# Performance work log

Hardware: AMD Instinct MI355X
Metric: run time of the kernel (lower is better)

## Reference

```python
import jax, jax.numpy as jnp
import numpy as np

IMG, PATCH, DIM, DEPTH, HEADS = 224, 16, 768, 12, 12
GRID = IMG // PATCH            # 14 patches per side
NPATCH = GRID * GRID           # 196
N = NPATCH + 1                 # 197 tokens incl. cls
HD = DIM // HEADS              # 64
NRD = (2 * GRID - 1) ** 2 + 3  # 732 relative-distance entries (incl. 3 cls slots)
FF = 4 * DIM                   # 3072
BATCH = 32


def _rel_pos_index():
    # Faithful port of the torch buffer construction (with_cls_token=True).
    coords = np.stack(np.meshgrid(np.arange(GRID), np.arange(GRID), indexing='ij'))
    cf = coords.reshape(2, -1)                                   # [2, 196]
    rel = (cf[:, :, None] - cf[:, None, :]).transpose(1, 2, 0)   # [196,196,2]
    rel = rel.astype(np.int64)
    rel[:, :, 0] += GRID - 1
    rel[:, :, 1] += GRID - 1
    rel[:, :, 0] *= 2 * GRID - 1
    rpi = np.zeros((N, N), dtype=np.int32)
    rpi[1:, 1:] = rel.sum(-1)
    rpi[0, :] = NRD - 3
    rpi[:, 0] = NRD - 2
    rpi[0, 0] = NRD - 1
    return jnp.asarray(rpi)

RPI = _rel_pos_index()  # [197,197] int32, constant


def layernorm(x, w, b, eps=1e-5):
    mu = x.mean(-1, keepdims=True)
    var = x.var(-1, keepdims=True)  # biased, like torch LayerNorm
    return (x - mu) * jax.lax.rsqrt(var + eps) * w + b


def setup_inputs() -> dict:
    key = jax.random.key(0)
    ks = jax.random.split(key, 12)
    s = 0.02
    f32 = jnp.float32
    return {
        'x': jax.random.normal(ks[0], (BATCH, 3, IMG, IMG), f32),
        # PatchEmbed conv (stride == kernel) expressed as a matmul weight.
        'patch_w': jax.random.normal(ks[1], (DIM, 3 * PATCH * PATCH), f32) * s,
        'patch_b': jnp.zeros((DIM,), f32),
        'cls_token': jax.random.normal(ks[2], (1, 1, DIM), f32) * s,
        # Per-block params, stacked along depth for lax.scan.
        'norm1_w': jnp.ones((DEPTH, DIM), f32),
        'norm1_b': jnp.zeros((DEPTH, DIM), f32),
        'qkv_w': jax.random.normal(ks[3], (DEPTH, 3 * DIM, DIM), f32) * s,
        'q_bias': jax.random.normal(ks[4], (DEPTH, DIM), f32) * s,
        'v_bias': jax.random.normal(ks[5], (DEPTH, DIM), f32) * s,
        'rpb_table': jax.random.normal(ks[6], (DEPTH, NRD, HEADS), f32) * s,
        'proj_w': jax.random.normal(ks[7], (DEPTH, DIM, DIM), f32) * s,
        'proj_b': jnp.zeros((DEPTH, DIM), f32),
        'norm2_w': jnp.ones((DEPTH, DIM), f32),
        'norm2_b': jnp.zeros((DEPTH, DIM), f32),
        'fc1_w': jax.random.normal(ks[8], (DEPTH, FF, DIM), f32) * s,
        'fc1_b': jnp.zeros((DEPTH, FF), f32),
        'fc2_w': jax.random.normal(ks[9], (DEPTH, DIM, FF), f32) * s,
        'fc2_b': jnp.zeros((DEPTH, DIM), f32),
        'normf_w': jnp.ones((DIM,), f32),
        'normf_b': jnp.zeros((DIM,), f32),
    }


def reference(x, patch_w, patch_b, cls_token, norm1_w, norm1_b, qkv_w, q_bias, v_bias,
              rpb_table, proj_w, proj_b, norm2_w, norm2_b, fc1_w, fc1_b, fc2_w, fc2_b,
              normf_w, normf_b):
    B = x.shape[0]
    # Patch embed: stride==kernel conv == patchify + matmul.
    p = x.reshape(B, 3, GRID, PATCH, GRID, PATCH).transpose(0, 2, 4, 1, 3, 5)
    p = p.reshape(B, NPATCH, 3 * PATCH * PATCH)
    tokens = p @ patch_w.T + patch_b                              # [B,196,768]
    tokens = jnp.concatenate([jnp.broadcast_to(cls_token, (B, 1, DIM)), tokens], axis=1)
    scale = HD ** -0.5

    def block(h, params):
        (n1w, n1b, qw, qb, vb, rpt, pw, pb, n2w, n2b, f1w, f1b, f2w, f2b) = params
        y = layernorm(h, n1w, n1b)
        bias = jnp.concatenate([qb, jnp.zeros_like(vb), vb])      # k bias is zero
        qkv = (y @ qw.T + bias).reshape(B, N, 3, HEADS, HD).transpose(2, 0, 3, 1, 4)
        q, k, v = qkv[0] * scale, qkv[1], qkv[2]                  # [B,H,N,HD]
        attn = jnp.einsum('bhnd,bhmd->bhnm', q, k)                # [B,H,N,N]
        rpb = rpt[RPI]                                            # [N,N,H] gather
        attn = attn + rpb.transpose(2, 0, 1)[None]
        attn = jax.nn.softmax(attn, axis=-1)
        o = jnp.einsum('bhnm,bhmd->bnhd', attn, v).reshape(B, N, DIM)
        h = h + o @ pw.T + pb
        y = layernorm(h, n2w, n2b)
        y = jax.nn.gelu(y @ f1w.T + f1b, approximate=False)       # torch nn.GELU (erf)
        h = h + y @ f2w.T + f2b
        return h, None

    params = (norm1_w, norm1_b, qkv_w, q_bias, v_bias, rpb_table, proj_w, proj_b,
              norm2_w, norm2_b, fc1_w, fc1_b, fc2_w, fc2_b)
    tokens, _ = jax.lax.scan(block, tokens, params)
    return layernorm(tokens, normf_w, normf_b)                    # [B,197,768]
```

## Files before the change

kernel.cpp:

```cpp
#include <hip/hip_runtime.h>
#include <hip/hip_bf16.h>


#define B_     32
#define DIM_   768
#define N_     197
#define M_     (B_*N_)
#define NP_    196
#define MP_    (B_*NP_)
#define HEADS_ 12
#define HD_    64
#define FF_    3072
#define NRD_   732
#define QKV_   2304
#define DEPTH_ 12

typedef unsigned short u16;
typedef unsigned int   u32;
typedef __attribute__((ext_vector_type(4))) float    f32x4;
typedef __attribute__((ext_vector_type(8))) u16      ushort8;
typedef __attribute__((ext_vector_type(8))) __bf16   bf16x8;

__device__ __forceinline__ float b2f(u16 u) {
    return __builtin_bit_cast(float, ((u32)u) << 16);
}
__device__ __forceinline__ u16 f2b(float f) {
    u32 u = __builtin_bit_cast(u32, f);
    u32 r = u + 0x7fffu + ((u >> 16) & 1u);
    return (u16)(r >> 16);
}
__device__ __forceinline__ float lo16(u32 v) { return __builtin_bit_cast(float, v << 16); }
__device__ __forceinline__ float hi16(u32 v) { return __builtin_bit_cast(float, v & 0xffff0000u); }

__device__ __forceinline__ f32x4 mfma16(ushort8 a, ushort8 b, f32x4 c) {
    return __builtin_amdgcn_mfma_f32_16x16x32_bf16(
        __builtin_bit_cast(bf16x8, a), __builtin_bit_cast(bf16x8, b), c, 0, 0, 0);
}

__device__ __forceinline__ void gload16(const u16* g, u16* lds) {
    __builtin_amdgcn_global_load_lds(
        (const __attribute__((address_space(1))) void*)g,
        (__attribute__((address_space(3))) void*)lds, 16, 0, 0);
}

__global__ void cvt_k(const float* __restrict__ src, u16* __restrict__ dst, int n8) {
    int g = blockIdx.x * 256 + threadIdx.x;
    if (g >= n8) return;
    size_t o = (size_t)g * 8;
    float4 f0 = *(const float4*)(src + o);
    float4 f1 = *(const float4*)(src + o + 4);
    ushort8 r;
    r[0]=f2b(f0.x); r[1]=f2b(f0.y); r[2]=f2b(f0.z); r[3]=f2b(f0.w);
    r[4]=f2b(f1.x); r[5]=f2b(f1.y); r[6]=f2b(f1.z); r[7]=f2b(f1.w);
    *(ushort8*)(dst + o) = r;
}

#define SEG0 1769472
#define SEG1 589824
#define SEG2 2359296
#define SEG3 2359296
__global__ void cvt4_k(const float* __restrict__ s0, const float* __restrict__ s1,
                       const float* __restrict__ s2, const float* __restrict__ s3,
                       u16* __restrict__ dst) {
    int g = blockIdx.x * 256 + threadIdx.x;
    if (g >= (SEG0+SEG1+SEG2+SEG3)/8) return;
    size_t o = (size_t)g * 8;
    const float* src; size_t lo_;
    if (o < SEG0)             { src = s0; lo_ = o; }
    else if (o < SEG0+SEG1)   { src = s1; lo_ = o - SEG0; }
    else if (o < (size_t)SEG0+SEG1+SEG2) { src = s2; lo_ = o - SEG0 - SEG1; }
    else                      { src = s3; lo_ = o - SEG0 - SEG1 - SEG2; }
    float4 f0 = *(const float4*)(src + lo_);
    float4 f1 = *(const float4*)(src + lo_ + 4);
    ushort8 r;
    r[0]=f2b(f0.x); r[1]=f2b(f0.y); r[2]=f2b(f0.z); r[3]=f2b(f0.w);
    r[4]=f2b(f1.x); r[5]=f2b(f1.y); r[6]=f2b(f1.z); r[7]=f2b(f1.w);
    *(ushort8*)(dst + o) = r;
}

__global__ void patchify_k(const float* __restrict__ X, u16* __restrict__ P) {
    int idx = blockIdx.x * 256 + threadIdx.x;
    if (idx >= MP_ * DIM_) return;
    int row = idx / DIM_, k = idx - row * DIM_;
    int b = row / NP_, p = row - b * NP_;
    int gy = p / 14, gx = p - gy * 14;
    int c = k >> 8, r = k & 255;
    int py = r >> 4, px = r & 15;
    P[idx] = f2b(X[((b * 3 + c) * 224 + gy * 16 + py) * 224 + gx * 16 + px]);
}

__global__ void build_tokens_k(const float* __restrict__ P, const float* __restrict__ cls,
                               float* __restrict__ T) {
    int idx = blockIdx.x * 256 + threadIdx.x;
    if (idx >= M_ * DIM_) return;
    int row = idx / DIM_, c = idx - row * DIM_;
    int b = row / N_, t = row - b * N_;
    T[idx] = (t == 0) ? cls[c] : P[(size_t)(b * NP_ + t - 1) * DIM_ + c];
}

__global__ void qkvbias_all_k(const float* __restrict__ qb, const float* __restrict__ vb,
                              float* __restrict__ out) {
    int g = blockIdx.x * 256 + threadIdx.x;
    if (g >= DEPTH_ * QKV_) return;
    int l = g / QKV_, n = g - l * QKV_;
    out[g] = (n < DIM_) ? qb[l * DIM_ + n]
                        : (n < 2 * DIM_ ? 0.f : vb[l * DIM_ + n - 2 * DIM_]);
}

template <int OUTBF>
__global__ void layernorm_k(const float* __restrict__ X, const float* __restrict__ w,
                            const float* __restrict__ bta, void* __restrict__ Yv) {
    int row = blockIdx.x;
    const float* x = X + (size_t)row * DIM_;
    int t = threadIdx.x;
    float v[3]; float s = 0.f, q = 0.f;
#pragma unroll
    for (int i = 0; i < 3; i++) { float u = x[t + i * 256]; v[i] = u; s += u; q += u * u; }
#pragma unroll
    for (int off = 32; off > 0; off >>= 1) {
        s += __shfl_down(s, off, 64);
        q += __shfl_down(q, off, 64);
    }
    __shared__ float ss[4], qq[4];
    int wid = t >> 6, lane = t & 63;
    if (!lane) { ss[wid] = s; qq[wid] = q; }
    __syncthreads();
    s = ss[0] + ss[1] + ss[2] + ss[3];
    q = qq[0] + qq[1] + qq[2] + qq[3];
    float mu = s * (1.f / 768.f);
    float var = q * (1.f / 768.f) - mu * mu;
    float rs = rsqrtf(var + 1e-5f);
#pragma unroll
    for (int i = 0; i < 3; i++) {
        int c = t + i * 256;
        float o = (v[i] - mu) * rs * w[c] + bta[c];
        if (OUTBF) ((u16*)Yv)[(size_t)row * DIM_ + c] = f2b(o);
        else       ((float*)Yv)[(size_t)row * DIM_ + c] = o;
    }
}

template <int ACT, int OUTBF>
__launch_bounds__(512)
__global__ void gemm_bt(const u16* __restrict__ A, const u16* __restrict__ W,
                        const float* __restrict__ bias, const float* res,
                        void* Cv, int M, int Nc, int K) {
    __shared__ u16 As[2][128 * 32];
    __shared__ u16 Ws[2][128 * 32];
    const int tid = threadIdx.x;
    const int lane = tid & 63, w = tid >> 6;
    const int llo = lane & 15, lhi = lane >> 4;
    const int wm = w & 3, wn = w >> 2;

    const int nwg = gridDim.x * gridDim.y;
    int bid = blockIdx.y * gridDim.x + blockIdx.x;
    {
        int q = nwg >> 3, r = nwg & 7;
        int xcd = bid & 7, idx = bid >> 3;
        bid = (xcd < r ? xcd * (q + 1) : r * (q + 1) + (xcd - r) * q) + idx;
    }
    const int m0 = (bid / gridDim.x) * 128, n0 = (bid % gridDim.x) * 128;

    f32x4 acc[2][4] = {};

    const int srow = tid >> 2, scol = (tid & 3) * 8;
    int ar = m0 + srow; if (ar >= M) ar = M - 1;
    const u16* ga = A + (size_t)ar * K + scol;
    const u16* gw = W + (size_t)(n0 + srow) * K + scol;
    const int ldso = (w * 16) * 32;

    gload16(ga, As[0] + ldso);
    gload16(gw, Ws[0] + ldso);
    __syncthreads();

    int cur = 0;
    for (int k0 = 32; k0 < K; k0 += 32) {
        const int nxt = cur ^ 1;
        gload16(ga + k0, As[nxt] + ldso);
        gload16(gw + k0, Ws[nxt] + ldso);
        ushort8 af[2], bfr[4];
#pragma unroll
        for (int mi = 0; mi < 2; mi++)
            af[mi] = *(const ushort8*)(As[cur] + (wm * 32 + mi * 16 + llo) * 32 + lhi * 8);
#pragma unroll
        for (int ni = 0; ni < 4; ni++)
            bfr[ni] = *(const ushort8*)(Ws[cur] + (wn * 64 + ni * 16 + llo) * 32 + lhi * 8);
#pragma unroll
        for (int mi = 0; mi < 2; mi++)
#pragma unroll
            for (int ni = 0; ni < 4; ni++)
                acc[mi][ni] = mfma16(af[mi], bfr[ni], acc[mi][ni]);
        __syncthreads();
        cur = nxt;
    }
    {
        ushort8 af[2], bfr[4];
#pragma unroll
        for (int mi = 0; mi < 2; mi++)
            af[mi] = *(const ushort8*)(As[cur] + (wm * 32 + mi * 16 + llo) * 32 + lhi * 8);
#pragma unroll
        for (int ni = 0; ni < 4; ni++)
            bfr[ni] = *(const ushort8*)(Ws[cur] + (wn * 64 + ni * 16 + llo) * 32 + lhi * 8);
#pragma unroll
        for (int mi = 0; mi < 2; mi++)
#pragma unroll
            for (int ni = 0; ni < 4; ni++)
                acc[mi][ni] = mfma16(af[mi], bfr[ni], acc[mi][ni]);
    }
    const int cb = n0 + wn * 64 + llo;
    const int rb = m0 + wm * 32 + lhi * 4;
#pragma unroll
    for (int ni = 0; ni < 4; ni++) {
        int col = cb + ni * 16;
        float bv = bias ? bias[col] : 0.f;
#pragma unroll
        for (int mi = 0; mi < 2; mi++) {
#pragma unroll
            for (int rg = 0; rg < 4; rg++) {
                int row = rb + mi * 16 + rg;
                if (row >= M) continue;
                float t = acc[mi][ni][rg] + bv;
                if (ACT) t = 0.5f * t * (1.f + erff(t * 0.70710678118654752f));
                if (res) t += res[(size_t)row * Nc + col];
                if (OUTBF) ((u16*)Cv)[(size_t)row * Nc + col] = f2b(t);
                else       ((float*)Cv)[(size_t)row * Nc + col] = t;
            }
        }
    }
}

__device__ __forceinline__ int vswz(int d) {
    return ((d & 7) ^ ((d >> 3) & 7)) << 3;
}

__launch_bounds__(256)
__global__ void attn3_k(const u16* __restrict__ qkv, const float* __restrict__ rpt,
                        u16* __restrict__ O) {
    __shared__ u16 smem[16128 + 16384];
    u16* Ks = smem;
    u16* Vt = smem + 16128;
    u16* Ps = smem;
    const int b = blockIdx.x / HEADS_, hh = blockIdx.x % HEADS_;
    const int i0 = blockIdx.y * 64;
    const int t = threadIdx.x;
    const int w = t >> 6, lane = t & 63;
    const int lhi = lane >> 4, llo = lane & 15;
    const size_t base = (size_t)b * N_ * QKV_ + (size_t)hh * HD_;
    const int iw = i0 + w * 16;

    int qrow = iw + llo; if (qrow > 196) qrow = 196;
    const ushort8 af0 = *(const ushort8*)(qkv + base + (size_t)qrow * QKV_ + lhi * 8);
    const ushort8 af1 = *(const ushort8*)(qkv + base + (size_t)qrow * QKV_ + 32 + lhi * 8);

    for (int g = t; g < 1576; g += 256) {
        int j = g >> 3, d0 = (g & 7) * 8;
        ushort8 kv = *(const ushort8*)(qkv + base + (size_t)j * QKV_ + 768 + d0);
        *(ushort8*)(Ks + j * 72 + d0) = kv;
        ushort8 vv = *(const ushort8*)(qkv + base + (size_t)j * QKV_ + 1536 + d0);
#pragma unroll
        for (int e = 0; e < 8; e++) {
            int d = d0 + e;
            Vt[d * 256 + (j ^ vswz(d))] = ((const u16*)&vv)[e];
        }
    }
    if (t < 216) {
        int j = 197 + (t >> 3), d0 = (t & 7) * 8;
        *(uint4*)(Ks + j * 72 + d0) = make_uint4(0u, 0u, 0u, 0u);
    }
    for (int g = t; g < 1728; g += 256) {
        int d = g / 27, c = 197 + (g - d * 27);
        Vt[d * 256 + (c ^ vswz(d))] = 0;
    }
    __syncthreads();

    const bool wvalid = (iw <= 196);
    f32x4 acc[14] = {};
    float mx[4], sum[4];

    if (wvalid) {
#pragma unroll
        for (int jt = 0; jt < 14; jt++) {
            const u16* kp = Ks + (jt * 16 + llo) * 72 + lhi * 8;
            ushort8 b0 = *(const ushort8*)(kp);
            ushort8 b1 = *(const ushort8*)(kp + 32);
            acc[jt] = mfma16(af0, b0, acc[jt]);
            acc[jt] = mfma16(af1, b1, acc[jt]);
        }
        int iy4[4], ix4[4]; bool icls[4];
#pragma unroll
        for (int rg = 0; rg < 4; rg++) {
            int i = iw + lhi * 4 + rg; if (i > 196) i = 196;
            icls[rg] = (i == 0);
            int pi = i - 1;
            iy4[rg] = pi / 14; ix4[rg] = pi - iy4[rg] * 14;
            mx[rg] = -INFINITY;
        }
#pragma unroll
        for (int jt = 0; jt < 14; jt++) {
            int j = jt * 16 + llo;
            if (j <= 196) {
                bool jcls = (j == 0);
                int pj = j - 1;
                int jy = pj / 14, jx = pj - jy * 14;
#pragma unroll
                for (int rg = 0; rg < 4; rg++) {
                    int idx;
                    if (icls[rg])  idx = jcls ? (NRD_ - 1) : (NRD_ - 3);
                    else if (jcls) idx = NRD_ - 2;
                    else           idx = (iy4[rg] - jy + 13) * 27 + (ix4[rg] - jx + 13);
                    float sv = acc[jt][rg] * 0.125f + rpt[idx * HEADS_ + hh];
                    acc[jt][rg] = sv;
                    mx[rg] = fmaxf(mx[rg], sv);
                }
            } else {
#pragma unroll
                for (int rg = 0; rg < 4; rg++) acc[jt][rg] = -INFINITY;
            }
        }
#pragma unroll
        for (int rg = 0; rg < 4; rg++) {
#pragma unroll
            for (int off = 1; off < 16; off <<= 1)
                mx[rg] = fmaxf(mx[rg], __shfl_xor(mx[rg], off, 64));
            sum[rg] = 0.f;
        }
#pragma unroll
        for (int jt = 0; jt < 14; jt++)
#pragma unroll
            for (int rg = 0; rg < 4; rg++) {
                float ev = __expf(acc[jt][rg] - mx[rg]);
                acc[jt][rg] = ev;
                sum[rg] += ev;
            }
#pragma unroll
        for (int rg = 0; rg < 4; rg++) {
#pragma unroll
            for (int off = 1; off < 16; off <<= 1)
                sum[rg] += __shfl_xor(sum[rg], off, 64);
            sum[rg] = 1.f / sum[rg];
        }
#pragma unroll
        for (int jt = 0; jt < 14; jt++)
#pragma unroll
            for (int rg = 0; rg < 4; rg++) acc[jt][rg] *= sum[rg];
    }
    __syncthreads();

    if (wvalid) {
#pragma unroll
        for (int jt = 0; jt < 14; jt++)
#pragma unroll
            for (int rg = 0; rg < 4; rg++)
                Ps[(w * 16 + lhi * 4 + rg) * 232 + jt * 16 + llo] = f2b(acc[jt][rg]);
        f32x4 o[4] = {};
#pragma unroll
        for (int jk = 0; jk < 7; jk++) {
            ushort8 pa = *(const ushort8*)(Ps + (w * 16 + llo) * 232 + jk * 32 + lhi * 8);
#pragma unroll
            for (int dt = 0; dt < 4; dt++) {
                int d = dt * 16 + llo;
                ushort8 vf = *(const ushort8*)(Vt + d * 256 + ((jk * 32 + lhi * 8) ^ vswz(d)));
                o[dt] = mfma16(pa, vf, o[dt]);
            }
        }
#pragma unroll
        for (int dt = 0; dt < 4; dt++)
#pragma unroll
            for (int rg = 0; rg < 4; rg++) {
                int i = iw + lhi * 4 + rg;
                if (i <= 196)
                    O[(size_t)(b * N_ + i) * DIM_ + hh * HD_ + dt * 16 + llo] = f2b(o[dt][rg]);
            }
    }
}

extern "C" void kernel_launch(void* const* d_in, const int* in_sizes, int n_in,
                              void* d_out, int out_size, void* d_ws, size_t ws_size,
                              hipStream_t stream) {
    (void)in_sizes; (void)n_in; (void)out_size; (void)ws_size;
    const float* x    = (const float*)d_in[0];
    const float* pew  = (const float*)d_in[1];
    const float* peb  = (const float*)d_in[2];
    const float* cls  = (const float*)d_in[3];
    const float* n1w  = (const float*)d_in[4];
    const float* n1b  = (const float*)d_in[5];
    const float* qkvw = (const float*)d_in[6];
    const float* qb   = (const float*)d_in[7];
    const float* vb   = (const float*)d_in[8];
    const float* rpt  = (const float*)d_in[9];
    const float* pw   = (const float*)d_in[10];
    const float* pb   = (const float*)d_in[11];
    const float* n2w  = (const float*)d_in[12];
    const float* n2b  = (const float*)d_in[13];
    const float* f1w  = (const float*)d_in[14];
    const float* f1b  = (const float*)d_in[15];
    const float* f2w  = (const float*)d_in[16];
    const float* f2b_ = (const float*)d_in[17];
    const float* nfw  = (const float*)d_in[18];
    const float* nfb  = (const float*)d_in[19];

    float* ws = (float*)d_ws;
    float* h     = ws;
    u16*   y     = (u16*)(ws + 4841472);
    float* un    = ws + 4841472 + 2420736;
    u16*   wbuf  = (u16*)(un + 9682944);
    float* qbias = (float*)(wbuf + 7077888);
    u16*   qkvb   = (u16*)un;
    u16*   hidden = (u16*)un;
    u16*   pmat   = (u16*)un;
    float* pout   = un + 4816896;

    const int MT = (M_ + 127) / 128;

    cvt_k<<<288, 256, 0, stream>>>(pew, wbuf, SEG1 / 8);
    patchify_k<<<(MP_ * DIM_ + 255) / 256, 256, 0, stream>>>(x, pmat);
    qkvbias_all_k<<<(DEPTH_ * QKV_ + 255) / 256, 256, 0, stream>>>(qb, vb, qbias);
    gemm_bt<0, 0><<<dim3(6, 49), 512, 0, stream>>>(pmat, wbuf, peb, nullptr, pout,
                                                   MP_, DIM_, DIM_);
    build_tokens_k<<<(M_ * DIM_ + 255) / 256, 256, 0, stream>>>(pout, cls, h);

    for (int l = 0; l < 12; l++) {
        layernorm_k<1><<<M_, 256, 0, stream>>>(h, n1w + l * DIM_, n1b + l * DIM_, y);
        cvt4_k<<<3456, 256, 0, stream>>>(qkvw + (size_t)l * SEG0, pw + (size_t)l * SEG1,
                                         f1w + (size_t)l * SEG2, f2w + (size_t)l * SEG3, wbuf);
        gemm_bt<0, 1><<<dim3(18, MT), 512, 0, stream>>>(y, wbuf, qbias + l * QKV_, nullptr,
                                                        qkvb, M_, QKV_, DIM_);
        attn3_k<<<dim3(384, 4), 256, 0, stream>>>(qkvb, rpt + (size_t)l * NRD_ * HEADS_, y);
        gemm_bt<0, 0><<<dim3(6, MT), 512, 0, stream>>>(y, wbuf + SEG0, pb + l * DIM_, h, h,
                                                       M_, DIM_, DIM_);
        layernorm_k<1><<<M_, 256, 0, stream>>>(h, n2w + l * DIM_, n2b + l * DIM_, y);
        gemm_bt<1, 1><<<dim3(24, MT), 512, 0, stream>>>(y, wbuf + SEG0 + SEG1, f1b + l * FF_,
                                                        nullptr, hidden, M_, FF_, DIM_);
        gemm_bt<0, 0><<<dim3(6, MT), 512, 0, stream>>>(hidden, wbuf + SEG0 + SEG1 + SEG2,
                                                       f2b_ + l * DIM_, h, h, M_, DIM_, FF_);
    }
    layernorm_k<0><<<M_, 256, 0, stream>>>(h, nfw, nfb, d_out);
}
```

Measured before the change: 3.573 ms.

## Deepen GEMM LDS pipeline to four stages and swizzle LDS layout

```diff
diff --git a/kernel.cpp b/kernel.cpp
--- a/kernel.cpp
+++ b/kernel.cpp
@@ -144,8 +144,8 @@
 __global__ void gemm_bt(const u16* __restrict__ A, const u16* __restrict__ W,
                         const float* __restrict__ bias, const float* res,
                         void* Cv, int M, int Nc, int K) {
-    __shared__ u16 As[2][128 * 32];
-    __shared__ u16 Ws[2][128 * 32];
+    __shared__ u16 As[4][128 * 32];
+    __shared__ u16 Ws[4][128 * 32];
     const int tid = threadIdx.x;
     const int lane = tid & 63, w = tid >> 6;
     const int llo = lane & 15, lhi = lane >> 4;
@@ -162,50 +162,50 @@
 
     f32x4 acc[2][4] = {};
 
-    const int srow = tid >> 2, scol = (tid & 3) * 8;
+    const int srow = tid >> 2;
+    const int scol = ((tid & 3) ^ ((srow >> 1) & 3)) * 8;
     int ar = m0 + srow; if (ar >= M) ar = M - 1;
     const u16* ga = A + (size_t)ar * K + scol;
     const u16* gw = W + (size_t)(n0 + srow) * K + scol;
     const int ldso = (w * 16) * 32;
 
-    gload16(ga, As[0] + ldso);
-    gload16(gw, Ws[0] + ldso);
-    __syncthreads();
-
-    int cur = 0;
-    for (int k0 = 32; k0 < K; k0 += 32) {
-        const int nxt = cur ^ 1;
-        gload16(ga + k0, As[nxt] + ldso);
-        gload16(gw + k0, Ws[nxt] + ldso);
+    const int rslot = (lhi ^ ((llo >> 1) & 3)) * 8;
+
+    const int nt = K >> 5;
+
+#pragma unroll
+    for (int p = 0; p < 3; ++p) {
+        gload16(ga + p * 32, As[p] + ldso);
+        gload16(gw + p * 32, Ws[p] + ldso);
+    }
+
+    for (int t = 0; t < nt; ++t) {
+        if (t < nt - 2)      asm volatile("s_waitcnt vmcnt(4)" ::: "memory");
+        else if (t < nt - 1) asm volatile("s_waitcnt vmcnt(2)" ::: "memory");
+        else                 asm volatile("s_waitcnt vmcnt(0)" ::: "memory");
+        __builtin_amdgcn_s_barrier();
+
+        const u16* ab = As[t & 3];
+        const u16* wb = Ws[t & 3];
         ushort8 af[2], bfr[4];
 #pragma unroll
         for (int mi = 0; mi < 2; mi++)
-            af[mi] = *(const ushort8*)(As[cur] + (wm * 32 + mi * 16 + llo) * 32 + lhi * 8);
+            af[mi] = *(const ushort8*)(ab + (wm * 32 + mi * 16 + llo) * 32 + rslot);
 #pragma unroll
         for (int ni = 0; ni < 4; ni++)
-            bfr[ni] = *(const ushort8*)(Ws[cur] + (wn * 64 + ni * 16 + llo) * 32 + lhi * 8);
+            bfr[ni] = *(const ushort8*)(wb + (wn * 64 + ni * 16 + llo) * 32 + rslot);
 #pragma unroll
         for (int mi = 0; mi < 2; mi++)
 #pragma unroll
             for (int ni = 0; ni < 4; ni++)
                 acc[mi][ni] = mfma16(af[mi], bfr[ni], acc[mi][ni]);
-        __syncthreads();
-        cur = nxt;
-    }
-    {
-        ushort8 af[2], bfr[4];
-#pragma unroll
-        for (int mi = 0; mi < 2; mi++)
-            af[mi] = *(const ushort8*)(As[cur] + (wm * 32 + mi * 16 + llo) * 32 + lhi * 8);
-#pragma unroll
-        for (int ni = 0; ni < 4; ni++)
-            bfr[ni] = *(const ushort8*)(Ws[cur] + (wn * 64 + ni * 16 + llo) * 32 + lhi * 8);
-#pragma unroll
-        for (int mi = 0; mi < 2; mi++)
-#pragma unroll
-            for (int ni = 0; ni < 4; ni++)
-                acc[mi][ni] = mfma16(af[mi], bfr[ni], acc[mi][ni]);
-    }
+
+        if (t + 3 < nt) {
+            gload16(ga + (size_t)(t + 3) * 32, As[(t + 3) & 3] + ldso);
+            gload16(gw + (size_t)(t + 3) * 32, Ws[(t + 3) & 3] + ldso);
+        }
+    }
+
     const int cb = n0 + wn * 64 + llo;
     const int rb = m0 + wm * 32 + lhi * 4;
 #pragma unroll
```

Result: faster. 3.447 ms (-3.6%).
